# Performance work log

Hardware: AMD Instinct MI355X
Metric: run time of the kernel (lower is better)

Reference implementation:

```python
import jax, jax.numpy as jnp
import numpy as np

T = 2048          # tokens (single causal sequence)
HID = 4096        # hidden_size
H = 32            # num_heads
DQ = 256          # per-head q/k dim (192 nope + 64 rope)
DN = 192          # nope dim
DR = 64           # rope dim
DV = 256          # v head dim
DKV = 512         # kv latent rank
QLORA = 2048      # q lora rank
EPS = 1e-6
THETA = 10000.0
SCALE = DQ ** -0.5


def rmsnorm(x, w):
    return x * jax.lax.rsqrt(jnp.mean(x * x, axis=-1, keepdims=True) + EPS) * w


def rope_neox(pos, x):
    # x: [T, h, DR]; neox style: rotate concatenated halves
    inv_freq = 1.0 / (THETA ** (jnp.arange(0, DR, 2, dtype=jnp.float32) / DR))  # [DR/2]
    ang = pos.astype(jnp.float32)[:, None] * inv_freq  # [T, DR/2]
    cos = jnp.cos(ang)[:, None, :]
    sin = jnp.sin(ang)[:, None, :]
    x1, x2 = jnp.split(x, 2, axis=-1)
    return jnp.concatenate([x1 * cos - x2 * sin, x2 * cos + x1 * sin], axis=-1)


def setup_inputs() -> dict:
    key = jax.random.key(0)
    ks = jax.random.split(key, 8)
    s = 0.02
    return {
        "hidden_states": jax.random.normal(ks[0], (T, HID), dtype=jnp.float32),
        "positions": jnp.arange(T, dtype=jnp.int32),
        "wq_a": jax.random.normal(ks[1], (HID, QLORA), dtype=jnp.float32) * s,
        "q_a_ln_w": jnp.ones((QLORA,), dtype=jnp.float32),
        "wq_b": jax.random.normal(ks[2], (QLORA, H * DQ), dtype=jnp.float32) * s,
        "wkv_a": jax.random.normal(ks[3], (HID, DKV + DR), dtype=jnp.float32) * s,
        "kv_a_ln_w": jnp.ones((DKV,), dtype=jnp.float32),
        "wkv_b": jax.random.normal(ks[4], (DKV, H * (DN + DV)), dtype=jnp.float32) * s,
        "wo": jax.random.normal(ks[5], (H * DV, HID), dtype=jnp.float32) * s,
    }


def reference(hidden_states, positions, wq_a, q_a_ln_w, wq_b, wkv_a, kv_a_ln_w, wkv_b, wo):
    # q path: lora down -> rmsnorm -> up -> [T, H, 256]
    q = rmsnorm(hidden_states @ wq_a, q_a_ln_w)
    q = (q @ wq_b).reshape(T, H, DQ)
    # kv path: latent 512 + shared k_pe 64
    latent = hidden_states @ wkv_a
    kv_a, k_pe = jnp.split(latent, [DKV], axis=-1)
    kv_a = rmsnorm(kv_a, kv_a_ln_w)
    kv = (kv_a @ wkv_b).reshape(T, H, DN + DV)
    k_nope, v = jnp.split(kv, [DN], axis=-1)
    q_nope, q_pe = jnp.split(q, [DN], axis=-1)
    k_pe = k_pe.reshape(T, 1, DR)
    q_pe = rope_neox(positions, q_pe)
    k_pe = rope_neox(positions, k_pe)
    q = jnp.concatenate([q_nope, q_pe], axis=-1)                       # [T, H, 256]
    k = jnp.concatenate([k_nope, jnp.broadcast_to(k_pe, (T, H, DR))], axis=-1)
    # causal attention
    scores = jnp.einsum("thd,shd->hts", q, k) * SCALE                  # [H, T, T]
    causal = jnp.tril(jnp.ones((T, T), dtype=bool))
    scores = jnp.where(causal[None], scores, jnp.finfo(scores.dtype).min)
    attn = jax.nn.softmax(scores, axis=-1)
    out = jnp.einsum("hts,shd->thd", attn, v).reshape(T, H * DV)
    return out @ wo
```

## Files before the change

kernel.cpp:

```cpp
#include <hip/hip_runtime.h>
#include <cstdint>
#include <cstddef>

#define T_    2048
#define HID_  4096
#define NH_   32
#define DQ_   256
#define DN_   192
#define DR_   64
#define DV_   256
#define DKV_  512
#define QL_   2048
#define NKV_  576
#define HDQ_  8192
#define HDKV_ 14336
#define HDV_  8192
#define SCALE_ 0.0625f
#define MN5_  8388608
#define SK5_  2
#define NKC_  2816
#define PS1_  5767168
#define SK1_  4

using bf16x8 = __attribute__((ext_vector_type(8))) short;
using f32x4  = __attribute__((ext_vector_type(4))) float;

__device__ ushort g_hb   [(size_t)T_*HID_];
__device__ ushort g_wtc  [(size_t)NKC_*HID_];
__device__ ushort g_wtqb [(size_t)HDQ_*QL_];
__device__ ushort g_wtkvb[(size_t)HDKV_*DKV_];
__device__ ushort g_wto  [(size_t)HID_*HDV_];
__device__ float  g_qa   [(size_t)T_*QL_];
__device__ ushort g_qn   [(size_t)T_*QL_];
__device__ ushort g_q    [(size_t)T_*HDQ_];
__device__ ushort g_kvn  [(size_t)T_*DKV_];
__device__ ushort g_kpe  [(size_t)T_*DR_];
__device__ ushort g_kv   [(size_t)T_*HDKV_];
__device__ ushort g_k    [(size_t)NH_*T_*DQ_];
__device__ ushort g_vt   [(size_t)NH_*DV_*T_];
__device__ ushort g_o    [(size_t)T_*HDV_];
__device__ float  g_p5   [(size_t)SK1_*PS1_];

__device__ __forceinline__ float b2f(ushort h){ union{unsigned u; float f;} x; x.u=((unsigned)h)<<16; return x.f; }
__device__ __forceinline__ ushort f2b(float f){ union{float f; unsigned u;} x; x.f=f; unsigned r=x.u + 0x7fffu + ((x.u>>16)&1u); return (ushort)(r>>16); }
__device__ __forceinline__ void storeC(float*  p, float v){ *p = v; }
__device__ __forceinline__ void storeC(ushort* p, float v){ *p = f2b(v); }

#define GLD16(gp, lp) __builtin_amdgcn_global_load_lds( \
    (const __attribute__((address_space(1))) unsigned*)(gp), \
    (__attribute__((address_space(3))) unsigned*)(lp), 16, 0, 0)

__global__ __launch_bounds__(256) void convert_hidden(const float* __restrict__ src) {
  size_t i = ((size_t)blockIdx.x*256 + threadIdx.x)*4;
  float4 v = *(const float4*)(src + i);
  ushort4 o; o.x=f2b(v.x); o.y=f2b(v.y); o.z=f2b(v.z); o.w=f2b(v.w);
  *(ushort4*)(g_hb + i) = o;
}

__global__ __launch_bounds__(256) void transpose_w(const float* __restrict__ W,
                                                   ushort* __restrict__ Wt,
                                                   int K, int N) {
  __shared__ float tile[64][33];
  const int bk = blockIdx.x*64, bn = blockIdx.y*32;
  const int tx = threadIdx.x & 31, ty = threadIdx.x >> 5;
  for (int r = ty; r < 64; r += 8) {
    int n = bn + tx;
    tile[r][tx] = (n < N) ? W[(size_t)(bk + r)*N + n] : 0.f;
  }
  __syncthreads();
  for (int rr = ty; rr < 32; rr += 8) {
    int n = bn + rr;
    unsigned pv = (unsigned)f2b(tile[2*tx][rr]) | ((unsigned)f2b(tile[2*tx+1][rr]) << 16);
    ((unsigned*)(Wt + (size_t)n*K))[(bk>>1) + tx] = pv;
  }
}

template<typename OutT, int S>
__global__ __launch_bounds__(512, 2) void gemm8(const ushort* __restrict__ A,
                                                const ushort* __restrict__ Bt,
                                                OutT* __restrict__ C,
                                                int M, int N, int Kfull, int pstride) {
  __shared__ ushort sm[65536];
  const int tid = threadIdx.x, lane = tid & 63, w = tid >> 6;
  const int wr = w >> 2, wc = w & 3, l15 = lane & 15, l4 = lane >> 4;
  const int swm = (l15 & 7) << 3;
  const int gm = M >> 8, gn = N >> 8;
  const int nb = gridDim.x, id = blockIdx.x;
  const int swz = (id & 7) * (nb >> 3) + (id >> 3);
  const int m0 = (swz % gm) << 8;
  const int rest = swz / gm;
  const int n0 = (rest % gn) << 8;
  const int ks = rest / gn;
  const int Ksl = Kfull / S;
  const int kofs = ks * Ksl;
  const int NT = Ksl >> 6;

#define STG_A(tt, qm) do { const int p_=(tt)&1, kb_=kofs+(tt)*64; \
    _Pragma("unroll") \
    for (int i_=0;i_<2;i_++){ \
      const int le_=(i_*512+tid)*8, r_=le_>>6, c_=le_&63; \
      const int tr_=(r_>>6)*128 + (qm)*64 + (r_&63); \
      GLD16(A + (size_t)(m0+tr_)*Kfull + kb_ + (c_ ^ ((r_&7)<<3)), \
            sm + p_*16384 + (qm)*8192 + le_); } } while(0)
#define STG_B(tt, qn) do { const int p_=(tt)&1, kb_=kofs+(tt)*64; \
    _Pragma("unroll") \
    for (int i_=0;i_<2;i_++){ \
      const int le_=(i_*512+tid)*8, r_=le_>>6, c_=le_&63; \
      const int tr_=(r_>>5)*64 + (qn)*32 + (r_&31); \
      GLD16(Bt + (size_t)(n0+tr_)*Kfull + kb_ + (c_ ^ ((r_&7)<<3)), \
            sm + 32768 + p_*16384 + (qn)*8192 + le_); } } while(0)

  f32x4 acc[8][4];
  #pragma unroll
  for (int i=0;i<8;i++)
    #pragma unroll
    for (int j=0;j<4;j++) acc[i][j] = f32x4{0.f,0.f,0.f,0.f};

  STG_A(0,0); STG_B(0,0); STG_A(0,1); STG_B(0,1);
  if (NT > 1) { STG_A(1,0); STG_B(1,0); }
  __builtin_amdgcn_sched_barrier(0);
  if (NT > 1) asm volatile("s_waitcnt vmcnt(4)" ::: "memory");
  else        asm volatile("s_waitcnt vmcnt(0)" ::: "memory");
  __builtin_amdgcn_sched_barrier(0);
  __builtin_amdgcn_s_barrier();

  for (int t = 0; t < NT; ++t) {
    const int p = t & 1;
    const ushort* Ab = sm + p*16384;
    const ushort* Bb = sm + 32768 + p*16384;
    bf16x8 af[4][2], bq0[2][2], bq1[2][2];

    #pragma unroll
    for (int mi=0;mi<4;mi++)
      #pragma unroll
      for (int k2=0;k2<2;k2++)
        af[mi][k2] = *(const bf16x8*)(Ab + (wr*64 + mi*16 + l15)*64 + ((k2*32 + 8*l4) ^ swm));
    #pragma unroll
    for (int nf=0;nf<2;nf++)
      #pragma unroll
      for (int k2=0;k2<2;k2++)
        bq0[nf][k2] = *(const bf16x8*)(Bb + (wc*32 + nf*16 + l15)*64 + ((k2*32 + 8*l4) ^ swm));
    if (t + 1 < NT) STG_A(t+1, 1);
    __builtin_amdgcn_sched_barrier(0);
    __builtin_amdgcn_s_barrier();
    __builtin_amdgcn_s_setprio(1);
    #pragma unroll
    for (int mi=0;mi<4;mi++)
      #pragma unroll
      for (int nf=0;nf<2;nf++)
        #pragma unroll
        for (int k2=0;k2<2;k2++)
          acc[mi][nf] = __builtin_amdgcn_mfma_f32_16x16x32_bf16(af[mi][k2], bq0[nf][k2], acc[mi][nf], 0,0,0);
    __builtin_amdgcn_s_setprio(0);
    __builtin_amdgcn_sched_barrier(0);
    __builtin_amdgcn_s_barrier();

    #pragma unroll
    for (int nf=0;nf<2;nf++)
      #pragma unroll
      for (int k2=0;k2<2;k2++)
        bq1[nf][k2] = *(const bf16x8*)(Bb + 8192 + (wc*32 + nf*16 + l15)*64 + ((k2*32 + 8*l4) ^ swm));
    if (t + 1 < NT) STG_B(t+1, 1);
    __builtin_amdgcn_sched_barrier(0);
    __builtin_amdgcn_s_barrier();
    __builtin_amdgcn_s_setprio(1);
    #pragma unroll
    for (int mi=0;mi<4;mi++)
      #pragma unroll
      for (int nf=0;nf<2;nf++)
        #pragma unroll
        for (int k2=0;k2<2;k2++)
          acc[mi][2+nf] = __builtin_amdgcn_mfma_f32_16x16x32_bf16(af[mi][k2], bq1[nf][k2], acc[mi][2+nf], 0,0,0);
    __builtin_amdgcn_s_setprio(0);
    __builtin_amdgcn_sched_barrier(0);
    __builtin_amdgcn_s_barrier();

    #pragma unroll
    for (int mi=0;mi<4;mi++)
      #pragma unroll
      for (int k2=0;k2<2;k2++)
        af[mi][k2] = *(const bf16x8*)(Ab + 8192 + (wr*64 + mi*16 + l15)*64 + ((k2*32 + 8*l4) ^ swm));
    if (t + 2 < NT) STG_A(t+2, 0);
    __builtin_amdgcn_sched_barrier(0);
    __builtin_amdgcn_s_barrier();
    __builtin_amdgcn_s_setprio(1);
    #pragma unroll
    for (int mi=0;mi<4;mi++)
      #pragma unroll
      for (int nf=0;nf<2;nf++)
        #pragma unroll
        for (int k2=0;k2<2;k2++)
          acc[4+mi][nf] = __builtin_amdgcn_mfma_f32_16x16x32_bf16(af[mi][k2], bq0[nf][k2], acc[4+mi][nf], 0,0,0);
    __builtin_amdgcn_s_setprio(0);
    __builtin_amdgcn_sched_barrier(0);
    __builtin_amdgcn_s_barrier();

    if (t + 2 < NT) STG_B(t+2, 0);
    __builtin_amdgcn_sched_barrier(0);
    if (t + 2 < NT)      asm volatile("s_waitcnt vmcnt(4)" ::: "memory");
    else if (t + 1 < NT) asm volatile("s_waitcnt vmcnt(0)" ::: "memory");
    __builtin_amdgcn_sched_barrier(0);
    __builtin_amdgcn_s_barrier();
    __builtin_amdgcn_s_setprio(1);
    #pragma unroll
    for (int mi=0;mi<4;mi++)
      #pragma unroll
      for (int nf=0;nf<2;nf++)
        #pragma unroll
        for (int k2=0;k2<2;k2++)
          acc[4+mi][2+nf] = __builtin_amdgcn_mfma_f32_16x16x32_bf16(af[mi][k2], bq1[nf][k2], acc[4+mi][2+nf], 0,0,0);
    __builtin_amdgcn_s_setprio(0);
    __builtin_amdgcn_sched_barrier(0);
    __builtin_amdgcn_s_barrier();
  }
#undef STG_A
#undef STG_B
  asm volatile("s_waitcnt vmcnt(0)" ::: "memory");

  #pragma unroll
  for (int mi=0;mi<8;mi++)
    #pragma unroll
    for (int nj=0;nj<4;nj++) {
      const int row = m0 + wr*128 + mi*16 + l4*4;
      const int col = n0 + wc*64 + nj*16 + l15;
      #pragma unroll
      for (int r=0;r<4;r++) {
        if (S == 1) storeC(&C[(size_t)(row+r)*N + col], acc[mi][nj][r]);
        else ((float*)C)[(size_t)ks*pstride + (size_t)(row+r)*N + col] = acc[mi][nj][r];
      }
    }
}

__global__ __launch_bounds__(256) void reduce5(const float* __restrict__ p, float* __restrict__ out) {
  size_t i = ((size_t)blockIdx.x*256 + threadIdx.x)*4;
  float4 a = *(const float4*)(p + i);
  #pragma unroll
  for (int s=1; s<SK5_; s++) {
    float4 b = *(const float4*)(p + (size_t)s*MN5_ + i);
    a.x+=b.x; a.y+=b.y; a.z+=b.z; a.w+=b.w;
  }
  *(float4*)(out + i) = a;
}

__global__ __launch_bounds__(256) void rmsnorm_q(const float* __restrict__ p,
                                                 const float* __restrict__ wln) {
  const int row = blockIdx.x;
  const float* x = p + (size_t)row*NKC_;
  float* xo = g_qa + (size_t)row*QL_;
  float ss = 0.f;
  for (int i = threadIdx.x; i < QL_/4; i += 256) {
    float4 v = *(const float4*)(x + i*4);
    #pragma unroll
    for (int s=1; s<SK1_; s++) {
      float4 b = *(const float4*)(x + (size_t)s*PS1_ + i*4);
      v.x+=b.x; v.y+=b.y; v.z+=b.z; v.w+=b.w;
    }
    ((float4*)xo)[i] = v;
    ss += v.x*v.x + v.y*v.y + v.z*v.z + v.w*v.w;
  }
  #pragma unroll
  for (int o=32;o>=1;o>>=1) ss += __shfl_xor(ss, o);
  __shared__ float sr[4];
  if ((threadIdx.x & 63) == 0) sr[threadIdx.x>>6] = ss;
  __syncthreads();
  float rs = rsqrtf((sr[0]+sr[1]+sr[2]+sr[3])/(float)QL_ + 1e-6f);
  for (int i = threadIdx.x; i < QL_; i += 256)
    g_qn[(size_t)row*QL_ + i] = f2b(xo[i]*rs*wln[i]);
}

__global__ __launch_bounds__(256) void kv_norm_rope(const float* __restrict__ p,
                                                    const float* __restrict__ wln,
                                                    const int* __restrict__ pos) {
  const int t = blockIdx.x;
  const float* base = p + (size_t)t*NKC_ + QL_;
  __shared__ float lat[NKV_];
  float ss = 0.f;
  for (int i = threadIdx.x; i < NKV_; i += 256) {
    float v = base[i];
    #pragma unroll
    for (int s=1; s<SK1_; s++) v += base[(size_t)s*PS1_ + i];
    lat[i] = v;
    if (i < DKV_) ss += v*v;
  }
  #pragma unroll
  for (int o=32;o>=1;o>>=1) ss += __shfl_xor(ss, o);
  __shared__ float sr[4];
  if ((threadIdx.x & 63) == 0) sr[threadIdx.x>>6] = ss;
  __syncthreads();
  float rs = rsqrtf((sr[0]+sr[1]+sr[2]+sr[3])/(float)DKV_ + 1e-6f);
  for (int i = threadIdx.x; i < DKV_; i += 256)
    g_kvn[(size_t)t*DKV_ + i] = f2b(lat[i]*rs*wln[i]);
  if (threadIdx.x < 32) {
    const int i = threadIdx.x;
    float pp = (float)pos[t];
    float ang = pp * powf(10000.f, -(float)i/32.f);
    float c = cosf(ang), s = sinf(ang);
    float x1 = lat[DKV_ + i], x2 = lat[DKV_ + 32 + i];
    g_kpe[(size_t)t*DR_ + i]      = f2b(x1*c - x2*s);
    g_kpe[(size_t)t*DR_ + 32 + i] = f2b(x2*c + x1*s);
  }
}

__global__ __launch_bounds__(256) void q_rope(const int* __restrict__ pos) {
  const int t = blockIdx.x;
  __shared__ float cs[32], sn[32];
  if (threadIdx.x < 32) {
    const int i = threadIdx.x;
    float p = (float)pos[t];
    float ang = p * powf(10000.f, -(float)i/32.f);
    cs[i] = cosf(ang); sn[i] = sinf(ang);
  }
  __syncthreads();
  for (int e = threadIdx.x; e < NH_*32; e += 256) {
    const int h = e >> 5, i = e & 31;
    ushort* qp = g_q + (size_t)t*HDQ_ + h*DQ_ + DN_;
    float x1 = b2f(qp[i]), x2 = b2f(qp[32 + i]);
    qp[i]      = f2b(x1*cs[i] - x2*sn[i]);
    qp[32 + i] = f2b(x2*cs[i] + x1*sn[i]);
  }
}

__global__ __launch_bounds__(256) void build_k() {
  const int t = blockIdx.x;
  for (int e = threadIdx.x; e < NH_*32; e += 256) {
    const int h = e >> 5, d = (e & 31)*8;
    uint4 v;
    if (d < DN_) v = *(const uint4*)(g_kv  + (size_t)t*HDKV_ + h*448 + d);
    else         v = *(const uint4*)(g_kpe + (size_t)t*DR_ + (d - DN_));
    *(uint4*)(g_k + ((size_t)h*T_ + t)*DQ_ + d) = v;
  }
}

__global__ __launch_bounds__(256) void build_vt() {
  const int h = blockIdx.x, tt = blockIdx.y;
  __shared__ ushort tile[64*272];
  const int tid = threadIdx.x;
  #pragma unroll
  for (int p=0;p<8;p++) {
    int le = (p*256+tid)*8;
    int tl = le >> 8, d = le & 255;
    uint4 v = *(const uint4*)(g_kv + (size_t)(tt*64 + tl)*HDKV_ + h*448 + DN_ + d);
    *(uint4*)(tile + tl*272 + d) = v;
  }
  __syncthreads();
  #pragma unroll
  for (int p=0;p<8;p++) {
    int le = (p*256+tid)*8;
    int d = le >> 6, tl0 = le & 63;
    ushort tmp[8];
    #pragma unroll
    for (int j=0;j<8;j++) tmp[j] = tile[(tl0+j)*272 + d];
    *(uint4*)(g_vt + ((size_t)h*DV_ + d)*T_ + tt*64 + tl0) = *(const uint4*)tmp;
  }
}

__global__ __launch_bounds__(256) void attn_kernel() {
  __shared__ ushort KV[64*256];
  __shared__ ushort Pl[4][16][64];
  const int h = blockIdx.x;
  const int qt = (gridDim.y - 1) - blockIdx.y;
  const int tid = threadIdx.x, lane = tid & 63, w = tid >> 6;
  const int l15 = lane & 15, l4 = lane >> 4;
  const int swm = (l15 & 7) << 3;

  const ushort* Kh = g_k  + (size_t)h*T_*DQ_;
  const ushort* Vh = g_vt + (size_t)h*DV_*T_;

#define STAGE_K(kt_) do { \
    const ushort* ks_ = Kh + (size_t)(kt_)*64*DQ_; \
    _Pragma("unroll") \
    for (int c_=0;c_<8;c_++){ int le_=(c_*256+tid)*8, r_=le_>>8, co_=le_&255; \
      GLD16(ks_ + r_*256 + (co_ ^ ((r_&7)<<3)), KV+le_); } } while(0)
#define STAGE_V(kt_) do { \
    _Pragma("unroll") \
    for (int c_=0;c_<8;c_++){ int le_=(c_*256+tid)*8, d_=le_>>6, kv_=le_&63; \
      GLD16(Vh + (size_t)d_*T_ + (kt_)*64 + (kv_ ^ ((d_&7)<<3)), KV+le_); } } while(0)

  const int q0 = qt*64;
  const int qrow = q0 + w*16 + l15;

  bf16x8 qf[8];
  {
    const ushort* qb = g_q + (size_t)qrow*HDQ_ + h*DQ_;
    #pragma unroll
    for (int g=0; g<8; g++) qf[g] = *(const bf16x8*)(qb + 32*g + 8*l4);
  }
  f32x4 acc[16];
  #pragma unroll
  for (int i=0;i<16;i++) acc[i] = f32x4{0.f,0.f,0.f,0.f};
  float m_r = -1e30f, l_r = 0.f;

  STAGE_K(0);

  for (int kt = 0; kt <= qt; ++kt) {
    __builtin_amdgcn_sched_barrier(0);
    asm volatile("s_waitcnt vmcnt(0)" ::: "memory");
    __builtin_amdgcn_sched_barrier(0);
    __builtin_amdgcn_s_barrier();

    f32x4 s[4];
    #pragma unroll
    for (int fn=0; fn<4; fn++) s[fn] = f32x4{0.f,0.f,0.f,0.f};
    __builtin_amdgcn_s_setprio(1);
    #pragma unroll
    for (int g=0; g<8; g++)
      #pragma unroll
      for (int fn=0; fn<4; fn++) {
        bf16x8 kf = *(const bf16x8*)(KV + (fn*16 + l15)*256 + ((32*g + 8*l4) ^ swm));
        s[fn] = __builtin_amdgcn_mfma_f32_16x16x32_bf16(kf, qf[g], s[fn], 0,0,0);
      }
    __builtin_amdgcn_s_setprio(0);
    asm volatile("s_waitcnt lgkmcnt(0)" ::: "memory");
    __builtin_amdgcn_sched_barrier(0);
    __builtin_amdgcn_s_barrier();
    STAGE_V(kt);
    __builtin_amdgcn_sched_barrier(0);

    if (kt == qt) {
      #pragma unroll
      for (int fn=0; fn<4; fn++)
        #pragma unroll
        for (int r=0;r<4;r++) {
          int kv = kt*64 + fn*16 + l4*4 + r;
          if (kv > qrow) s[fn][r] = -1e30f;
        }
    }

    float mx = s[0][0];
    #pragma unroll
    for (int fn=0; fn<4; fn++)
      #pragma unroll
      for (int r=0;r<4;r++) mx = fmaxf(mx, s[fn][r]);
    mx = fmaxf(mx, __shfl_xor(mx, 16));
    mx = fmaxf(mx, __shfl_xor(mx, 32));
    mx *= SCALE_;
    if (__any(mx > m_r)) {
      float mn = fmaxf(m_r, mx);
      float sc = __expf(m_r - mn);
      m_r = mn;
      l_r *= sc;
      #pragma unroll
      for (int fd=0; fd<16; fd++)
        #pragma unroll
        for (int r=0;r<4;r++) acc[fd][r] *= sc;
    }
    float ssum = 0.f;
    #pragma unroll
    for (int fn=0; fn<4; fn++)
      #pragma unroll
      for (int r=0;r<4;r++) {
        float p = __expf(fmaf(s[fn][r], SCALE_, -m_r));
        s[fn][r] = p; ssum += p;
      }
    ssum += __shfl_xor(ssum, 16);
    ssum += __shfl_xor(ssum, 32);
    l_r += ssum;

    #pragma unroll
    for (int fn=0; fn<4; fn++) {
      ushort4 pw;
      pw.x = f2b(s[fn][0]); pw.y = f2b(s[fn][1]);
      pw.z = f2b(s[fn][2]); pw.w = f2b(s[fn][3]);
      *(ushort4*)(&Pl[w][l15][(fn*16 + l4*4) ^ swm]) = pw;
    }

    __builtin_amdgcn_sched_barrier(0);
    asm volatile("s_waitcnt vmcnt(0)" ::: "memory");
    __builtin_amdgcn_sched_barrier(0);
    __builtin_amdgcn_s_barrier();

    __builtin_amdgcn_s_setprio(1);
    #pragma unroll
    for (int s2=0; s2<2; s2++) {
      bf16x8 pa = *(const bf16x8*)(&Pl[w][l15][(s2*32 + 8*l4) ^ swm]);
      #pragma unroll
      for (int fd=0; fd<16; fd++) {
        bf16x8 vb = *(const bf16x8*)(KV + (fd*16 + l15)*64 + ((s2*32 + 8*l4) ^ swm));
        acc[fd] = __builtin_amdgcn_mfma_f32_16x16x32_bf16(vb, pa, acc[fd], 0,0,0);
      }
    }
    __builtin_amdgcn_s_setprio(0);
    asm volatile("s_waitcnt lgkmcnt(0)" ::: "memory");
    __builtin_amdgcn_sched_barrier(0);
    __builtin_amdgcn_s_barrier();
    if (kt < qt) STAGE_K(kt+1);
    __builtin_amdgcn_sched_barrier(0);
  }

  l_r = 1.f / l_r;
  #pragma unroll
  for (int fd=0; fd<16; fd++) {
    ushort4 ow;
    ow.x = f2b(acc[fd][0] * l_r); ow.y = f2b(acc[fd][1] * l_r);
    ow.z = f2b(acc[fd][2] * l_r); ow.w = f2b(acc[fd][3] * l_r);
    *(ushort4*)(g_o + (size_t)qrow*HDV_ + h*DV_ + fd*16 + l4*4) = ow;
  }
#undef STAGE_K
#undef STAGE_V
}

extern "C" void kernel_launch(void* const* d_in, const int* in_sizes, int n_in,
                              void* d_out, int out_size, void* d_ws, size_t ws_size,
                              hipStream_t stream) {
  (void)in_sizes; (void)n_in; (void)d_ws; (void)ws_size; (void)out_size;
  const float* hs    = (const float*)d_in[0];
  const int*   pos   = (const int*)  d_in[1];
  const float* wqa   = (const float*)d_in[2];
  const float* qlnw  = (const float*)d_in[3];
  const float* wqb   = (const float*)d_in[4];
  const float* wkva  = (const float*)d_in[5];
  const float* kvlnw = (const float*)d_in[6];
  const float* wkvb  = (const float*)d_in[7];
  const float* wo    = (const float*)d_in[8];
  float* out = (float*)d_out;

  void *p_hb, *p_wtc, *p_wtqb, *p_wtkvb, *p_wto;
  void *p_qn, *p_q, *p_kvn, *p_kv, *p_o, *p_p5;
  hipGetSymbolAddress(&p_hb,    HIP_SYMBOL(g_hb));
  hipGetSymbolAddress(&p_wtc,   HIP_SYMBOL(g_wtc));
  hipGetSymbolAddress(&p_wtqb,  HIP_SYMBOL(g_wtqb));
  hipGetSymbolAddress(&p_wtkvb, HIP_SYMBOL(g_wtkvb));
  hipGetSymbolAddress(&p_wto,   HIP_SYMBOL(g_wto));
  hipGetSymbolAddress(&p_qn,    HIP_SYMBOL(g_qn));
  hipGetSymbolAddress(&p_q,     HIP_SYMBOL(g_q));
  hipGetSymbolAddress(&p_kvn,   HIP_SYMBOL(g_kvn));
  hipGetSymbolAddress(&p_kv,    HIP_SYMBOL(g_kv));
  hipGetSymbolAddress(&p_o,     HIP_SYMBOL(g_o));
  hipGetSymbolAddress(&p_p5,    HIP_SYMBOL(g_p5));

  convert_hidden<<<8192, 256, 0, stream>>>(hs);
  transpose_w<<<dim3(HID_/64,  QL_/32),        256, 0, stream>>>(wqa,  (ushort*)p_wtc,                        HID_, QL_);
  transpose_w<<<dim3(HID_/64, (NKC_-QL_)/32),  256, 0, stream>>>(wkva, (ushort*)p_wtc + (size_t)QL_*HID_,     HID_, NKV_);
  transpose_w<<<dim3(QL_/64,   HDQ_/32),       256, 0, stream>>>(wqb,  (ushort*)p_wtqb,  QL_,  HDQ_);
  transpose_w<<<dim3(DKV_/64,  HDKV_/32),      256, 0, stream>>>(wkvb, (ushort*)p_wtkvb, DKV_, HDKV_);
  transpose_w<<<dim3(HDV_/64,  HID_/32),       256, 0, stream>>>(wo,   (ushort*)p_wto,   HDV_, HID_);

  gemm8<float,SK1_><<<(T_/256)*(NKC_/256)*SK1_, 512, 0, stream>>>((const ushort*)p_hb, (const ushort*)p_wtc, (float*)p_p5, T_, NKC_, HID_, PS1_);
  rmsnorm_q<<<T_, 256, 0, stream>>>((const float*)p_p5, qlnw);
  kv_norm_rope<<<T_, 256, 0, stream>>>((const float*)p_p5, kvlnw, pos);

  gemm8<ushort,1><<<(T_/256)*(HDQ_/256), 512, 0, stream>>>((const ushort*)p_qn, (const ushort*)p_wtqb, (ushort*)p_q, T_, HDQ_, QL_, 0);
  q_rope<<<T_, 256, 0, stream>>>(pos);
  gemm8<ushort,1><<<(T_/256)*(HDKV_/256), 512, 0, stream>>>((const ushort*)p_kvn, (const ushort*)p_wtkvb, (ushort*)p_kv, T_, HDKV_, DKV_, 0);

  build_k<<<T_, 256, 0, stream>>>();
  build_vt<<<dim3(NH_, T_/64), 256, 0, stream>>>();
  attn_kernel<<<dim3(NH_, 32), 256, 0, stream>>>();

  gemm8<float,SK5_><<<(T_/256)*(HID_/256)*SK5_, 512, 0, stream>>>((const ushort*)p_o, (const ushort*)p_wto, (float*)p_p5, T_, HID_, HDV_, MN5_);
  reduce5<<<MN5_/1024, 256, 0, stream>>>((const float*)p_p5, out);
}
```

Measured before the change: 756.1 us.

## Fuse q rope into attention and k assembly into kv GEMM epilogue

Removes the q_rope and build_k kernels. The kv up-projection GEMM epilogue now writes k_nope straight into the per-head K buffer and keeps v in g_kv. kv_norm_rope broadcasts the rotated k_pe into every head's K rows, and the attention kernel applies rope to its Q fragments in registers after loading them. This saves two launches and a full read and rewrite of Q and K. In exchange it adds scattered, less coalesced 2-byte stores in the GEMM epilogue and recomputes the trig functions in every attention block.

```diff
diff --git a/kernel.cpp b/kernel.cpp
--- a/kernel.cpp
+++ b/kernel.cpp
@@ -34,7 +34,6 @@
 __device__ ushort g_qn   [(size_t)T_*QL_];
 __device__ ushort g_q    [(size_t)T_*HDQ_];
 __device__ ushort g_kvn  [(size_t)T_*DKV_];
-__device__ ushort g_kpe  [(size_t)T_*DR_];
 __device__ ushort g_kv   [(size_t)T_*HDKV_];
 __device__ ushort g_k    [(size_t)NH_*T_*DQ_];
 __device__ ushort g_vt   [(size_t)NH_*DV_*T_];
@@ -75,7 +74,7 @@
   }
 }
 
-template<typename OutT, int S>
+template<typename OutT, int S, int EPI>
 __global__ __launch_bounds__(512, 2) void gemm8(const ushort* __restrict__ A,
                                                 const ushort* __restrict__ Bt,
                                                 OutT* __restrict__ C,
@@ -223,10 +222,20 @@
     for (int nj=0;nj<4;nj++) {
       const int row = m0 + wr*128 + mi*16 + l4*4;
       const int col = n0 + wc*64 + nj*16 + l15;
-      #pragma unroll
-      for (int r=0;r<4;r++) {
-        if (S == 1) storeC(&C[(size_t)(row+r)*N + col], acc[mi][nj][r]);
-        else ((float*)C)[(size_t)ks*pstride + (size_t)(row+r)*N + col] = acc[mi][nj][r];
+      if (EPI == 2) {
+        const int h = col / 448, j = col - h*448;
+        #pragma unroll
+        for (int r=0;r<4;r++) {
+          ushort v = f2b(acc[mi][nj][r]);
+          if (j < DN_) g_k[((size_t)h*T_ + row + r)*DQ_ + j] = v;
+          else         g_kv[(size_t)(row + r)*HDKV_ + col]   = v;
+        }
+      } else {
+        #pragma unroll
+        for (int r=0;r<4;r++) {
+          if (S == 1) storeC(&C[(size_t)(row+r)*N + col], acc[mi][nj][r]);
+          else ((float*)C)[(size_t)ks*pstride + (size_t)(row+r)*N + col] = acc[mi][nj][r];
+        }
       }
     }
 }
@@ -290,44 +299,20 @@
   float rs = rsqrtf((sr[0]+sr[1]+sr[2]+sr[3])/(float)DKV_ + 1e-6f);
   for (int i = threadIdx.x; i < DKV_; i += 256)
     g_kvn[(size_t)t*DKV_ + i] = f2b(lat[i]*rs*wln[i]);
-  if (threadIdx.x < 32) {
-    const int i = threadIdx.x;
+  {
+    const int i = threadIdx.x & 31, hb = threadIdx.x >> 5;
     float pp = (float)pos[t];
     float ang = pp * powf(10000.f, -(float)i/32.f);
     float c = cosf(ang), s = sinf(ang);
     float x1 = lat[DKV_ + i], x2 = lat[DKV_ + 32 + i];
-    g_kpe[(size_t)t*DR_ + i]      = f2b(x1*c - x2*s);
-    g_kpe[(size_t)t*DR_ + 32 + i] = f2b(x2*c + x1*s);
-  }
-}
-
-__global__ __launch_bounds__(256) void q_rope(const int* __restrict__ pos) {
-  const int t = blockIdx.x;
-  __shared__ float cs[32], sn[32];
-  if (threadIdx.x < 32) {
-    const int i = threadIdx.x;
-    float p = (float)pos[t];
-    float ang = p * powf(10000.f, -(float)i/32.f);
-    cs[i] = cosf(ang); sn[i] = sinf(ang);
-  }
-  __syncthreads();
-  for (int e = threadIdx.x; e < NH_*32; e += 256) {
-    const int h = e >> 5, i = e & 31;
-    ushort* qp = g_q + (size_t)t*HDQ_ + h*DQ_ + DN_;
-    float x1 = b2f(qp[i]), x2 = b2f(qp[32 + i]);
-    qp[i]      = f2b(x1*cs[i] - x2*sn[i]);
-    qp[32 + i] = f2b(x2*cs[i] + x1*sn[i]);
-  }
-}
-
-__global__ __launch_bounds__(256) void build_k() {
-  const int t = blockIdx.x;
-  for (int e = threadIdx.x; e < NH_*32; e += 256) {
-    const int h = e >> 5, d = (e & 31)*8;
-    uint4 v;
-    if (d < DN_) v = *(const uint4*)(g_kv  + (size_t)t*HDKV_ + h*448 + d);
-    else         v = *(const uint4*)(g_kpe + (size_t)t*DR_ + (d - DN_));
-    *(uint4*)(g_k + ((size_t)h*T_ + t)*DQ_ + d) = v;
+    ushort k1 = f2b(x1*c - x2*s);
+    ushort k2 = f2b(x2*c + x1*s);
+    #pragma unroll
+    for (int hh = 0; hh < 4; ++hh) {
+      const int h = hb + hh*8;
+      g_k[((size_t)h*T_ + t)*DQ_ + DN_ + i]      = k1;
+      g_k[((size_t)h*T_ + t)*DQ_ + DN_ + 32 + i] = k2;
+    }
   }
 }
 
@@ -354,7 +339,7 @@
   }
 }
 
-__global__ __launch_bounds__(256) void attn_kernel() {
+__global__ __launch_bounds__(256) void attn_kernel(const int* __restrict__ pos) {
   __shared__ ushort KV[64*256];
   __shared__ ushort Pl[4][16][64];
   const int h = blockIdx.x;
@@ -384,6 +369,16 @@
     const ushort* qb = g_q + (size_t)qrow*HDQ_ + h*DQ_;
     #pragma unroll
     for (int g=0; g<8; g++) qf[g] = *(const bf16x8*)(qb + 32*g + 8*l4);
+    float pp = (float)pos[qrow];
+    #pragma unroll
+    for (int e=0; e<8; ++e) {
+      const int i = 8*l4 + e;
+      float ang = pp * powf(10000.f, -(float)i/32.f);
+      float c = cosf(ang), s = sinf(ang);
+      float x1 = b2f((ushort)qf[6][e]), x2 = b2f((ushort)qf[7][e]);
+      qf[6][e] = (short)f2b(x1*c - x2*s);
+      qf[7][e] = (short)f2b(x2*c + x1*s);
+    }
   }
   f32x4 acc[16];
   #pragma unroll
@@ -535,18 +530,16 @@
   transpose_w<<<dim3(DKV_/64,  HDKV_/32),      256, 0, stream>>>(wkvb, (ushort*)p_wtkvb, DKV_, HDKV_);
   transpose_w<<<dim3(HDV_/64,  HID_/32),       256, 0, stream>>>(wo,   (ushort*)p_wto,   HDV_, HID_);
 
-  gemm8<float,SK1_><<<(T_/256)*(NKC_/256)*SK1_, 512, 0, stream>>>((const ushort*)p_hb, (const ushort*)p_wtc, (float*)p_p5, T_, NKC_, HID_, PS1_);
+  gemm8<float,SK1_,1><<<(T_/256)*(NKC_/256)*SK1_, 512, 0, stream>>>((const ushort*)p_hb, (const ushort*)p_wtc, (float*)p_p5, T_, NKC_, HID_, PS1_);
   rmsnorm_q<<<T_, 256, 0, stream>>>((const float*)p_p5, qlnw);
   kv_norm_rope<<<T_, 256, 0, stream>>>((const float*)p_p5, kvlnw, pos);
 
-  gemm8<ushort,1><<<(T_/256)*(HDQ_/256), 512, 0, stream>>>((const ushort*)p_qn, (const ushort*)p_wtqb, (ushort*)p_q, T_, HDQ_, QL_, 0);
-  q_rope<<<T_, 256, 0, stream>>>(pos);
-  gemm8<ushort,1><<<(T_/256)*(HDKV_/256), 512, 0, stream>>>((const ushort*)p_kvn, (const ushort*)p_wtkvb, (ushort*)p_kv, T_, HDKV_, DKV_, 0);
-
-  build_k<<<T_, 256, 0, stream>>>();
+  gemm8<ushort,1,0><<<(T_/256)*(HDQ_/256), 512, 0, stream>>>((const ushort*)p_qn, (const ushort*)p_wtqb, (ushort*)p_q, T_, HDQ_, QL_, 0);
+  gemm8<ushort,1,2><<<(T_/256)*(HDKV_/256), 512, 0, stream>>>((const ushort*)p_kvn, (const ushort*)p_wtkvb, (ushort*)p_kv, T_, HDKV_, DKV_, 0);
+
   build_vt<<<dim3(NH_, T_/64), 256, 0, stream>>>();
-  attn_kernel<<<dim3(NH_, 32), 256, 0, stream>>>();
-
-  gemm8<float,SK5_><<<(T_/256)*(HID_/256)*SK5_, 512, 0, stream>>>((const ushort*)p_o, (const ushort*)p_wto, (float*)p_p5, T_, HID_, HDV_, MN5_);
+  attn_kernel<<<dim3(NH_, 32), 256, 0, stream>>>(pos);
+
+  gemm8<float,SK5_,1><<<(T_/256)*(HID_/256)*SK5_, 512, 0, stream>>>((const ushort*)p_o, (const ushort*)p_wto, (float*)p_p5, T_, HID_, HDV_, MN5_);
   reduce5<<<MN5_/1024, 256, 0, stream>>>((const float*)p_p5, out);
 }
```

Measured after the change: 801.0 us. +5.9%, slower.
